# Performance work log

Hardware: AMD Instinct MI355X
Metric: run time of the kernel (lower is better)

Reference implementation:

```python
import jax, jax.numpy as jnp
import numpy as np

M, D, G, E = 100000, 64, 1024, 1600000  # nodes, hidden, graphs, edges


def setup_inputs() -> dict:
    key = jax.random.key(0)
    k1, k2, k3, k4 = jax.random.split(key, 4)
    x = jax.random.normal(k1, (M, D), dtype=jnp.float32)
    batch = jnp.sort(jax.random.randint(k2, (M,), 0, G)).astype(jnp.int64)
    edge = jax.random.randint(k3, (2, E), 0, M).astype(jnp.int64)
    # nn.Linear(D, 1) parameters
    att_w = jax.random.normal(k4, (1, D), dtype=jnp.float32) * (1.0 / np.sqrt(D))
    att_b = jnp.zeros((1,), dtype=jnp.float32)
    return {"x": x, "att_w": att_w, "att_b": att_b, "batch": batch, "edge": edge}


def reference(x, att_w, att_b, batch, edge):
    # imp = attention(x): [M, 1] -> [M]
    imp = (x @ att_w.T + att_b)[:, 0]
    # scatter_softmax of imp over graph segments (batch)
    seg_max = jax.ops.segment_max(imp, batch, num_segments=G)
    e = jnp.exp(imp - seg_max[batch])
    denom = jax.ops.segment_sum(e, batch, num_segments=G)
    a = e / denom[batch]  # [M]
    # (degree branch is dead code when degree=False; degree softmax unused)
    # per-node weighted outer product imp_k * x_k x_k^T, scatter-summed per graph
    wj = (a[:, None] * x)[:, :, None] * x[:, None, :]  # [M, D, D]
    out = jax.ops.segment_sum(wj, batch, num_segments=G)  # [G, D, D]
    # Triuvec: upper-triangular (incl. diagonal) vectorization, row-major
    iu = jnp.triu_indices(D)
    return out[:, iu[0], iu[1]]  # [G, D*(D+1)/2]
```

## Files before the change

kernel.cpp:

```cpp
#include <hip/hip_runtime.h>
#include <hip/hip_bf16.h>
#include <math.h>


#define DDIM 64
#define NTRI 2080
#define CAP  1024
#define TK   32

typedef __bf16 bf16x8 __attribute__((ext_vector_type(8)));
typedef float  f32x4  __attribute__((ext_vector_type(4)));

__device__ __forceinline__ float dot_row_w(const float* __restrict__ row,
                                           const float* __restrict__ sW) {
    float d = 0.f;
#pragma unroll
    for (int k = 0; k < 16; ++k) {
        const float4 v = ((const float4*)row)[k];
        const float4 w = ((const float4*)sW)[k];
        d = fmaf(v.x, w.x, d); d = fmaf(v.y, w.y, d);
        d = fmaf(v.z, w.z, d); d = fmaf(v.w, w.w, d);
    }
    return d;
}

__device__ __forceinline__ unsigned pack_bf16(float a, float b) {
    __hip_bfloat162 h2 = __float22bfloat162_rn(make_float2(a, b));
    return *reinterpret_cast<unsigned*>(&h2);
}

__global__ void __launch_bounds__(256)
bounds_kernel(const int* __restrict__ batch, int* __restrict__ seg_start, int M, int G)
{
    const int m = blockIdx.x * 256 + threadIdx.x;
    if (m >= M) return;
    const int b0 = batch[m];
    if (m == 0) {
        for (int g = 0; g <= b0; ++g) seg_start[g] = 0;
    } else {
        const int bp = batch[m - 1];
        for (int g = bp + 1; g <= b0; ++g) seg_start[g] = m;
    }
    if (m == M - 1) {
        for (int g = b0 + 1; g <= G; ++g) seg_start[g] = M;
    }
}

__global__ void __launch_bounds__(256)
sop_kernel(const float* __restrict__ x,
           const float* __restrict__ att_w,
           const float* __restrict__ att_b,
           const int*   __restrict__ seg_start,
           float*       __restrict__ out)
{
    __shared__ unsigned short sT[2][2][DDIM * TK];
    __shared__ float sA[CAP];
    __shared__ float sW[DDIM];
    __shared__ float sRed[8];

    const int g   = blockIdx.x;
    const int tid = threadIdx.x;
    const int s   = seg_start[g];
    const int n   = seg_start[g + 1] - s;
    float* og = out + (size_t)g * NTRI;

    if (n == 0) {
        for (int i = tid; i < NTRI; i += 256) og[i] = 0.f;
        return;
    }

    const float4* x4 = (const float4*)x;
    const int lane16 = tid & 15;
    const int grp16  = tid >> 4;

    const int pp = tid & 15;
    const int cc = tid >> 4;
    float4 p0, p1;
    {
        const int m0 = 2 * pp;
        const float4 z = {0.f, 0.f, 0.f, 0.f};
        p0 = (m0     < n) ? x4[(size_t)(s + m0) * 16 + cc]     : z;
        p1 = (m0 + 1 < n) ? x4[(size_t)(s + m0 + 1) * 16 + cc] : z;
    }

    const float4 wv = ((const float4*)att_w)[lane16];
    const float  bb = att_b[0];
    if (tid < DDIM) sW[tid] = att_w[tid];

    float lsum = 0.f;
    for (int idx = grp16; idx < n; idx += 16) {
        const float4 v = x4[(size_t)(s + idx) * 16 + lane16];
        float d = fmaf(v.x, wv.x, fmaf(v.y, wv.y, fmaf(v.z, wv.z, v.w * wv.w)));
        d += __shfl_xor(d, 1, 16);
        d += __shfl_xor(d, 2, 16);
        d += __shfl_xor(d, 4, 16);
        d += __shfl_xor(d, 8, 16);
        if (lane16 == 0) {
            const float e = __expf(d + bb);
            if (idx < CAP) sA[idx] = e;
            lsum += e;
        }
    }
    const int wid = tid >> 6, lane = tid & 63;
#pragma unroll
    for (int off = 32; off > 0; off >>= 1) lsum += __shfl_down(lsum, off, 64);
    if (lane == 0) sRed[wid] = lsum;
    __syncthreads();
    if (tid == 0) sRed[4] = 1.0f / (sRed[0] + sRed[1] + sRed[2] + sRed[3]);

    const int il = lane & 15;
    const int qd = lane >> 4;
    const int sw = qd ^ ((il >> 1) & 3);
    const int offA = (16 * wid + il) * TK + (sw << 3);
    const int offB = il * TK + (sw << 3);

    f32x4 acc[4];
#pragma unroll
    for (int jt = 0; jt < 4; ++jt) acc[jt] = (f32x4){0.f, 0.f, 0.f, 0.f};

    const int T = (n + TK - 1) / TK;

    for (int t = 0; t < T; ++t) {
        const int t0  = t * TK;
        const int cur = t & 1;
        unsigned* A32 = (unsigned*)sT[cur][0];
        unsigned* B32 = (unsigned*)sT[cur][1];

        const int m0 = t0 + 2 * pp;
        float c0 = 0.f, c1 = 0.f;
        if (m0 < n)
            c0 = (m0 < CAP) ? sA[m0]
               : __expf(dot_row_w(x + (size_t)(s + m0) * DDIM, sW) + bb);
        if (m0 + 1 < n)
            c1 = (m0 + 1 < CAP) ? sA[m0 + 1]
               : __expf(dot_row_w(x + (size_t)(s + m0 + 1) * DDIM, sW) + bb);

        const float* f0 = (const float*)&p0;
        const float* f1 = (const float*)&p1;
#pragma unroll
        for (int jf = 0; jf < 4; ++jf) {
            const int f   = 4 * cc + jf;
            const int pos = (pp >> 2) ^ ((f >> 1) & 3);
            const int ui  = f * (TK / 2) + (pos << 2) + (pp & 3);
            A32[ui] = pack_bf16(c0 * f0[jf], c1 * f1[jf]);
            B32[ui] = pack_bf16(f0[jf], f1[jf]);
        }

        if (t + 1 < T) {
            const int m0n = (t + 1) * TK + 2 * pp;
            const float4 z = {0.f, 0.f, 0.f, 0.f};
            p0 = (m0n     < n) ? x4[(size_t)(s + m0n) * 16 + cc]     : z;
            p1 = (m0n + 1 < n) ? x4[(size_t)(s + m0n + 1) * 16 + cc] : z;
        }
        __syncthreads();

        const unsigned short* As = sT[cur][0];
        const unsigned short* Bs = sT[cur][1];
        const bf16x8 av = *(const bf16x8*)(As + offA);
#pragma unroll
        for (int jt = 0; jt < 4; ++jt) {
            const bf16x8 bv = *(const bf16x8*)(Bs + offB + jt * 16 * TK);
            acc[jt] = __builtin_amdgcn_mfma_f32_16x16x32_bf16(av, bv, acc[jt], 0, 0, 0);
        }
    }

    const float invd = sRed[4];
    const int rbase = 16 * wid + qd * 4;
#pragma unroll
    for (int jt = 0; jt < 4; ++jt) {
        const int j = 16 * jt + il;
#pragma unroll
        for (int r = 0; r < 4; ++r) {
            const int i = rbase + r;
            if (j >= i) og[i * DDIM - (i * (i - 1)) / 2 + (j - i)] = acc[jt][r] * invd;
        }
    }
}

extern "C" void kernel_launch(void* const* d_in, const int* in_sizes, int n_in,
                              void* d_out, int out_size, void* d_ws, size_t ws_size,
                              hipStream_t stream) {
    const float* x     = (const float*)d_in[0];
    const float* att_w = (const float*)d_in[1];
    const float* att_b = (const float*)d_in[2];
    const int*   batch = (const int*)d_in[3];
    float* out = (float*)d_out;

    const int M = in_sizes[0] / DDIM;
    const int G = out_size / NTRI;

    int* seg_start = (int*)d_ws;

    bounds_kernel<<<(M + 255) / 256, 256, 0, stream>>>(batch, seg_start, M, G);
    sop_kernel<<<G, 256, 0, stream>>>(x, att_w, att_b, seg_start, out);
}
```

Measured before the change: 102.3 us.

## Fuse attention score computation into the single tiled pass over node rows

Removes the separate first pass over each graph's node rows that computed attention exponentials into shared memory. The scores are now computed from the same float4 fragments already loaded for the MFMA tile staging, using a 16-lane shuffle reduction, and the softmax denominator is reduced after the main loop. The thread-to-data mapping and LDS swizzle change to match, and the normalizer scales by 16 to undo the replicated per-lane sums. Halving global reads of x is the goal; in exchange there are extra shuffles inside the loop and an added barrier at the end.

```diff
diff --git a/kernel.cpp b/kernel.cpp
--- a/kernel.cpp
+++ b/kernel.cpp
@@ -5,24 +5,10 @@
 
 #define DDIM 64
 #define NTRI 2080
-#define CAP  1024
 #define TK   32
 
 typedef __bf16 bf16x8 __attribute__((ext_vector_type(8)));
 typedef float  f32x4  __attribute__((ext_vector_type(4)));
-
-__device__ __forceinline__ float dot_row_w(const float* __restrict__ row,
-                                           const float* __restrict__ sW) {
-    float d = 0.f;
-#pragma unroll
-    for (int k = 0; k < 16; ++k) {
-        const float4 v = ((const float4*)row)[k];
-        const float4 w = ((const float4*)sW)[k];
-        d = fmaf(v.x, w.x, d); d = fmaf(v.y, w.y, d);
-        d = fmaf(v.z, w.z, d); d = fmaf(v.w, w.w, d);
-    }
-    return d;
-}
 
 __device__ __forceinline__ unsigned pack_bf16(float a, float b) {
     __hip_bfloat162 h2 = __float22bfloat162_rn(make_float2(a, b));
@@ -54,8 +40,6 @@
            float*       __restrict__ out)
 {
     __shared__ unsigned short sT[2][2][DDIM * TK];
-    __shared__ float sA[CAP];
-    __shared__ float sW[DDIM];
     __shared__ float sRed[8];
 
     const int g   = blockIdx.x;
@@ -70,87 +54,66 @@
     }
 
     const float4* x4 = (const float4*)x;
-    const int lane16 = tid & 15;
-    const int grp16  = tid >> 4;
+    const int wid  = tid >> 6;
+    const int lane = tid & 63;
+    const int c    = lane & 15;
+    const int q    = lane >> 4;
+    const int p    = 4 * wid + q;
 
-    const int pp = tid & 15;
-    const int cc = tid >> 4;
-    float4 p0, p1;
-    {
-        const int m0 = 2 * pp;
-        const float4 z = {0.f, 0.f, 0.f, 0.f};
-        p0 = (m0     < n) ? x4[(size_t)(s + m0) * 16 + cc]     : z;
-        p1 = (m0 + 1 < n) ? x4[(size_t)(s + m0 + 1) * 16 + cc] : z;
-    }
+    const float4 wv = ((const float4*)att_w)[c];
+    const float  bb = att_b[0];
 
-    const float4 wv = ((const float4*)att_w)[lane16];
-    const float  bb = att_b[0];
-    if (tid < DDIM) sW[tid] = att_w[tid];
-
-    float lsum = 0.f;
-    for (int idx = grp16; idx < n; idx += 16) {
-        const float4 v = x4[(size_t)(s + idx) * 16 + lane16];
-        float d = fmaf(v.x, wv.x, fmaf(v.y, wv.y, fmaf(v.z, wv.z, v.w * wv.w)));
-        d += __shfl_xor(d, 1, 16);
-        d += __shfl_xor(d, 2, 16);
-        d += __shfl_xor(d, 4, 16);
-        d += __shfl_xor(d, 8, 16);
-        if (lane16 == 0) {
-            const float e = __expf(d + bb);
-            if (idx < CAP) sA[idx] = e;
-            lsum += e;
-        }
-    }
-    const int wid = tid >> 6, lane = tid & 63;
-#pragma unroll
-    for (int off = 32; off > 0; off >>= 1) lsum += __shfl_down(lsum, off, 64);
-    if (lane == 0) sRed[wid] = lsum;
-    __syncthreads();
-    if (tid == 0) sRed[4] = 1.0f / (sRed[0] + sRed[1] + sRed[2] + sRed[3]);
-
-    const int il = lane & 15;
-    const int qd = lane >> 4;
-    const int sw = qd ^ ((il >> 1) & 3);
-    const int offA = (16 * wid + il) * TK + (sw << 3);
-    const int offB = il * TK + (sw << 3);
+    const int sw   = q ^ ((c >> 2) & 3);
+    const int offA = (16 * wid + c) * TK + (sw << 3);
+    const int offB = c * TK + (sw << 3);
 
     f32x4 acc[4];
 #pragma unroll
     for (int jt = 0; jt < 4; ++jt) acc[jt] = (f32x4){0.f, 0.f, 0.f, 0.f};
 
     const int T = (n + TK - 1) / TK;
+    float lsum = 0.f;
+
+    float4 p0, p1;
+    {
+        const int m0 = 2 * p;
+        const float4 z = {0.f, 0.f, 0.f, 0.f};
+        p0 = (m0     < n) ? x4[(size_t)(s + m0) * 16 + c]     : z;
+        p1 = (m0 + 1 < n) ? x4[(size_t)(s + m0 + 1) * 16 + c] : z;
+    }
 
     for (int t = 0; t < T; ++t) {
-        const int t0  = t * TK;
+        const int m0  = t * TK + 2 * p;
         const int cur = t & 1;
+
+        float d0 = fmaf(p0.x, wv.x, fmaf(p0.y, wv.y, fmaf(p0.z, wv.z, p0.w * wv.w)));
+        float d1 = fmaf(p1.x, wv.x, fmaf(p1.y, wv.y, fmaf(p1.z, wv.z, p1.w * wv.w)));
+#pragma unroll
+        for (int mk = 1; mk < 16; mk <<= 1) {
+            d0 += __shfl_xor(d0, mk, 16);
+            d1 += __shfl_xor(d1, mk, 16);
+        }
+        float e0 = 0.f, e1 = 0.f;
+        if (m0     < n) e0 = __expf(d0 + bb);
+        if (m0 + 1 < n) e1 = __expf(d1 + bb);
+        lsum += e0 + e1;
+
         unsigned* A32 = (unsigned*)sT[cur][0];
         unsigned* B32 = (unsigned*)sT[cur][1];
-
-        const int m0 = t0 + 2 * pp;
-        float c0 = 0.f, c1 = 0.f;
-        if (m0 < n)
-            c0 = (m0 < CAP) ? sA[m0]
-               : __expf(dot_row_w(x + (size_t)(s + m0) * DDIM, sW) + bb);
-        if (m0 + 1 < n)
-            c1 = (m0 + 1 < CAP) ? sA[m0 + 1]
-               : __expf(dot_row_w(x + (size_t)(s + m0 + 1) * DDIM, sW) + bb);
-
         const float* f0 = (const float*)&p0;
         const float* f1 = (const float*)&p1;
 #pragma unroll
         for (int jf = 0; jf < 4; ++jf) {
-            const int f   = 4 * cc + jf;
-            const int pos = (pp >> 2) ^ ((f >> 1) & 3);
-            const int ui  = f * (TK / 2) + (pos << 2) + (pp & 3);
-            A32[ui] = pack_bf16(c0 * f0[jf], c1 * f1[jf]);
+            const int ui = (4 * c + jf) * 16 + ((wid ^ (c & 3)) << 2) + q;
+            A32[ui] = pack_bf16(e0 * f0[jf], e1 * f1[jf]);
             B32[ui] = pack_bf16(f0[jf], f1[jf]);
         }
 
         if (t + 1 < T) {
-            const int m0n = (t + 1) * TK + 2 * pp;
+            const int m0n = (t + 1) * TK + 2 * p;
             const float4 z = {0.f, 0.f, 0.f, 0.f};
-            p0 = (m0n     < n) ? x4[(size_t)(s + m0n) * 16 + cc]     : z;
-            p1 = (m0n + 1 < n) ? x4[(size_t)(s + m0n + 1) * 16 + cc] : z;
+            p0 = (m0n     < n) ? x4[(size_t)(s + m0n) * 16 + c]     : z;
+            p1 = (m0n + 1 < n) ? x4[(size_t)(s + m0n + 1) * 16 + c] : z;
         }
         __syncthreads();
 
@@ -164,11 +127,18 @@
         }
     }
 
+#pragma unroll
+    for (int off = 32; off > 0; off >>= 1) lsum += __shfl_down(lsum, off, 64);
+    if (lane == 0) sRed[wid] = lsum;
+    __syncthreads();
+    if (tid == 0) sRed[4] = 16.0f / (sRed[0] + sRed[1] + sRed[2] + sRed[3]);
+    __syncthreads();
     const float invd = sRed[4];
-    const int rbase = 16 * wid + qd * 4;
+
+    const int rbase = 16 * wid + q * 4;
 #pragma unroll
     for (int jt = 0; jt < 4; ++jt) {
-        const int j = 16 * jt + il;
+        const int j = 16 * jt + c;
 #pragma unroll
         for (int r = 0; r < 4; ++r) {
             const int i = rbase + r;
```

Result: faster. 90.77 us (-11.3%).
